# Kernel optimization log

Measured on AMD Instinct MI355X. Metric: run time of the kernel, lower is better.

The kernel has to match this reference:

```python
import jax, jax.numpy as jnp
import numpy as np

B, CIN, COUT, H, W = 4, 256, 256, 64, 64
K, G = 3, 4
PAD = (K - 1) // 2


def setup_inputs() -> dict:
    key = jax.random.key(0)
    k0, k1, k2, k3 = jax.random.split(key, 4)
    x = jax.random.normal(k0, (B, CIN, H, W), jnp.float32)
    y = jax.random.normal(k1, (B, 2, H, W), jnp.float32)
    # conv_offset: 1x1 conv, no bias, init std=0.1 (normal_init)
    w_offset = jax.random.normal(k2, (G * 2 * K * K, 2, 1, 1), jnp.float32) * 0.1
    # DeformConv2d weight, no bias, init std=0.01
    w_deform = jax.random.normal(k3, (COUT, CIN, K, K), jnp.float32) * 0.01
    return {"x": x, "y": y, "w_offset": w_offset, "w_deform": w_deform}


def _deform_conv(x, offset, weight):
    """DCN v1: stride 1, dilation 1, zero padding PAD, deform_groups=G, groups=1."""
    KK = K * K
    # mmcv offset layout: [B, G*2*KK, H, W] -> per group, per kernel pos, (dy, dx)
    off = offset.reshape(B, G, KK, 2, H, W)
    dy, dx = off[:, :, :, 0], off[:, :, :, 1]            # [B,G,KK,H,W]
    ii, jj = jnp.meshgrid(jnp.arange(K), jnp.arange(K), indexing="ij")
    ky = ii.reshape(KK).astype(x.dtype)                  # kernel row offsets
    kx = jj.reshape(KK).astype(x.dtype)                  # kernel col offsets
    base_y = jnp.arange(H, dtype=x.dtype)[None, :, None] - PAD + ky[:, None, None]  # [KK,H,1]
    base_x = jnp.arange(W, dtype=x.dtype)[None, None, :] - PAD + kx[:, None, None]  # [KK,1,W]
    yc = dy + base_y                                     # [B,G,KK,H,W]
    xc = dx + base_x

    Cg = CIN // G
    xg = x.reshape(B, G, Cg, H, W)

    def sample(xg1, yc1, xc1):
        # xg1 [Cg,H,W]; yc1/xc1 [KK,H,W] -> bilinear sample with zero padding
        y0 = jnp.floor(yc1)
        x0 = jnp.floor(xc1)
        wy = yc1 - y0
        wx = xc1 - x0
        y0i = y0.astype(jnp.int32)
        x0i = x0.astype(jnp.int32)

        def gather(yi, xi):
            valid = (yi >= 0) & (yi < H) & (xi >= 0) & (xi < W)
            v = xg1[:, jnp.clip(yi, 0, H - 1), jnp.clip(xi, 0, W - 1)]  # [Cg,KK,H,W]
            return v * valid[None].astype(xg1.dtype)

        v00 = gather(y0i, x0i)
        v01 = gather(y0i, x0i + 1)
        v10 = gather(y0i + 1, x0i)
        v11 = gather(y0i + 1, x0i + 1)
        return (v00 * (1 - wy) * (1 - wx) + v01 * (1 - wy) * wx
                + v10 * wy * (1 - wx) + v11 * wy * wx)

    sampled = jax.vmap(jax.vmap(sample))(xg, yc, xc)     # [B,G,Cg,KK,H,W]
    sampled = sampled.reshape(B, CIN, KK, H, W)
    wflat = weight.reshape(COUT, CIN, KK)
    return jnp.einsum("bckhw,ock->bohw", sampled, wflat)  # [B,COUT,H,W]


def reference(x, y, w_offset, w_deform):
    # offset = conv_offset(y.detach()), a 1x1 conv without bias
    y_det = jax.lax.stop_gradient(y)
    offset = jnp.einsum("bihw,oi->bohw", y_det, w_offset[:, :, 0, 0])
    out = _deform_conv(x, offset, w_deform)
    return jax.nn.relu(out)
```

## Files before the change

### kernel.cpp

```cpp
#include <hip/hip_runtime.h>
#include <cstddef>

#define B_    4
#define CIN_  256
#define COUT_ 256
#define H_    64
#define W_    64
#define KK_   9
#define G_    4
#define PAD_  1
#define TPX   64
#define NSL   9

#define WS_XT   0u
#define WS_WB   8388608u
#define WS_P23  9568256u

typedef short bf16x8 __attribute__((ext_vector_type(8)));
typedef float f32x4  __attribute__((ext_vector_type(4)));
typedef __attribute__((address_space(1))) const unsigned int* gptr_t;
typedef __attribute__((address_space(3))) unsigned int*       lptr_t;

__device__ __forceinline__ unsigned short f2bf(float v) {
    unsigned int u = __float_as_uint(v);
    u += 0x7fffu + ((u >> 16) & 1u);
    return (unsigned short)(u >> 16);
}
__device__ __forceinline__ float f_lo(unsigned int u) { return __uint_as_float(u << 16); }
__device__ __forceinline__ float f_hi(unsigned int u) { return __uint_as_float(u & 0xffff0000u); }

__global__ __launch_bounds__(256) void prep_kernel(const float* __restrict__ x,
                                                   const float* __restrict__ w,
                                                   unsigned short* __restrict__ xT,
                                                   unsigned short* __restrict__ wb) {
    const int tid = threadIdx.x;
    if (blockIdx.x < 512) {
        __shared__ unsigned short s[128][66];
        const int bh    = blockIdx.x >> 1;
        const int chalf = blockIdx.x & 1;
        const size_t src_base = ((size_t)(bh >> 6) * CIN_ + chalf * 128) * (H_ * W_) + (bh & 63) * W_;
        #pragma unroll 4
        for (int k = 0; k < 32; ++k) {
            int i = k * 256 + tid;
            int c = i >> 6, wq = i & 63;
            s[c][wq] = f2bf(x[src_base + (size_t)c * (H_ * W_) + wq]);
        }
        __syncthreads();
        #pragma unroll 4
        for (int k = 0; k < 16; ++k) {
            int j  = k * 256 + tid;
            int c2 = (j & 63) * 2, wq = j >> 6;
            unsigned int lo = s[c2][wq], hi = s[c2 + 1][wq];
            *(unsigned int*)(xT + ((size_t)bh * 64 + wq) * 256 + chalf * 128 + c2) = lo | (hi << 16);
        }
    } else {
        const int base = (blockIdx.x - 512) * 1024 + tid * 4;
        #pragma unroll
        for (int u = 0; u < 4; ++u) {
            int idx = base + u;
            int e   = idx & 7;
            int pos = (idx >> 3) & 7;
            int o   = (idx >> 6) & 255;
            int t   = idx >> 14;
            int g   = t / 9, kk = t - g * 9;
            int j   = pos ^ (o & 7);
            int c   = g * 64 + j * 8 + e;
            wb[idx] = f2bf(w[(o * CIN_ + c) * KK_ + kk]);
        }
    }
}

__global__ __launch_bounds__(512, 4) void dcn_kernel(
    const unsigned short* __restrict__ xT, const float* __restrict__ y,
    const float* __restrict__ w_off, const unsigned short* __restrict__ wb,
    unsigned int* __restrict__ outu,
    unsigned int* __restrict__ p23)
{
    __shared__ unsigned short s_W[COUT_ * 64];
    __shared__ unsigned short s_S[TPX * 64];

    const int tid = threadIdx.x;
    const int bid = blockIdx.x;
    const int kq  = bid & 3;
    const int bl  = (bid >> 2) & 1;
    const int loc = bid >> 3;
    const int h   = loc & 63;
    const int b   = (loc >> 6) * 2 + bl;

    const int sp = tid & 63;
    const int c8 = tid >> 6;

    const float yv0 = y[((b * 2 + 0) * H_ + h) * W_ + sp];
    const float yv1 = y[((b * 2 + 1) * H_ + h) * W_ + sp];

    const int lane = tid & 63, wave = tid >> 6;
    const int pg  = wave & 1, oh = wave >> 1;
    const int l15 = lane & 15, kq4 = lane >> 4, sw = l15 & 7;

    f32x4 acc[8];
    #pragma unroll
    for (int i = 0; i < 8; ++i) acc[i] = (f32x4){0.f, 0.f, 0.f, 0.f};

    const size_t xbase = (size_t)b * (H_ * W_ * 256) + c8 * 8;

    for (int sl = 0; sl < NSL; ++sl) {
        const int s  = kq * NSL + sl;
        const int kk = sl;

        __syncthreads();

        {
            const unsigned short* src = wb + (size_t)s * 16384;
            #pragma unroll
            for (int j = 0; j < 4; ++j) {
                const int off = (j * 512 + tid) * 8;
                __builtin_amdgcn_global_load_lds((gptr_t)(src + off),
                                                 (lptr_t)(s_W + off), 16, 0, 0);
            }
        }

        {
            const float4 co = *(const float4*)(w_off + s * 4);
            const float dy = fmaf(yv0, co.x, yv1 * co.y);
            const float dx = fmaf(yv0, co.z, yv1 * co.w);
            const float yc = (float)(h + (kk / 3) - PAD_) + dy;
            const float xc = (float)(sp + (kk % 3) - PAD_) + dx;
            const float yf = floorf(yc), xf = floorf(xc);
            const float wy = yc - yf,    wx = xc - xf;
            const int   yi = (int)yf,    xi = (int)xf;
            float w00 = (1.f - wy) * (1.f - wx);
            float w01 = (1.f - wy) * wx;
            float w10 = wy * (1.f - wx);
            float w11 = wy * wx;
            const bool y0ok = (yi >= 0) & (yi < H_);
            const bool y1ok = (yi >= -1) & (yi < H_ - 1);
            const bool x0ok = (xi >= 0) & (xi < W_);
            const bool x1ok = (xi >= -1) & (xi < W_ - 1);
            w00 = (y0ok & x0ok) ? w00 : 0.f;
            w01 = (y0ok & x1ok) ? w01 : 0.f;
            w10 = (y1ok & x0ok) ? w10 : 0.f;
            w11 = (y1ok & x1ok) ? w11 : 0.f;
            const int y0c = min(max(yi, 0), H_ - 1);
            const int y1c = min(max(yi + 1, 0), H_ - 1);
            const int x0c = min(max(xi, 0), W_ - 1);
            const int x1c = min(max(xi + 1, 0), W_ - 1);
            const unsigned short* xb = xT + xbase + kq * 64;
            const uint4 A  = *(const uint4*)(xb + ((size_t)y0c * W_ + x0c) * 256);
            const uint4 Bv = *(const uint4*)(xb + ((size_t)y0c * W_ + x1c) * 256);
            const uint4 C  = *(const uint4*)(xb + ((size_t)y1c * W_ + x0c) * 256);
            const uint4 D  = *(const uint4*)(xb + ((size_t)y1c * W_ + x1c) * 256);
            const unsigned int av[4] = {A.x, A.y, A.z, A.w};
            const unsigned int bv[4] = {Bv.x, Bv.y, Bv.z, Bv.w};
            const unsigned int cv[4] = {C.x, C.y, C.z, C.w};
            const unsigned int dv[4] = {D.x, D.y, D.z, D.w};
            unsigned int res[4];
            #pragma unroll
            for (int q = 0; q < 4; ++q) {
                float rl = w00 * f_lo(av[q]);
                rl = fmaf(w01, f_lo(bv[q]), rl);
                rl = fmaf(w10, f_lo(cv[q]), rl);
                rl = fmaf(w11, f_lo(dv[q]), rl);
                float rh = w00 * f_hi(av[q]);
                rh = fmaf(w01, f_hi(bv[q]), rh);
                rh = fmaf(w10, f_hi(cv[q]), rh);
                rh = fmaf(w11, f_hi(dv[q]), rh);
                res[q] = __builtin_amdgcn_perm(__float_as_uint(rh),
                                               __float_as_uint(rl), 0x07060302u);
            }
            *(uint4*)(s_S + sp * 64 + ((c8 ^ (sp & 7)) * 8)) =
                make_uint4(res[0], res[1], res[2], res[3]);
        }

        __syncthreads();

        bf16x8 bf[2][2], af[2][4];
        #pragma unroll
        for (int kh = 0; kh < 2; ++kh) {
            const int pos = ((kh * 4 + kq4) ^ sw) * 8;
            #pragma unroll
            for (int nt = 0; nt < 2; ++nt)
                bf[kh][nt] = *(const bf16x8*)(s_S + (pg * 32 + nt * 16 + l15) * 64 + pos);
            #pragma unroll
            for (int mt = 0; mt < 4; ++mt)
                af[kh][mt] = *(const bf16x8*)(s_W + (oh * 64 + mt * 16 + l15) * 64 + pos);
        }
        #pragma unroll
        for (int kh = 0; kh < 2; ++kh)
            #pragma unroll
            for (int nt = 0; nt < 2; ++nt)
                #pragma unroll
                for (int mt = 0; mt < 4; ++mt)
                    acc[nt * 4 + mt] = __builtin_amdgcn_mfma_f32_16x16x32_bf16(
                        af[kh][mt], bf[kh][nt], acc[nt * 4 + mt], 0, 0, 0);
    }

    unsigned short* pdst = (unsigned short*)((kq < 2) ? outu : p23) + (kq & 1);
    #pragma unroll
    for (int nt = 0; nt < 2; ++nt) {
        const int px = pg * 32 + nt * 16 + l15;
        #pragma unroll
        for (int mt = 0; mt < 4; ++mt) {
            const int obase = oh * 64 + mt * 16 + kq4 * 4;
            #pragma unroll
            for (int r = 0; r < 4; ++r) {
                const size_t gi = (((size_t)b * COUT_ + obase + r) * H_ + h) * W_ + px;
                pdst[gi * 2] = f2bf(acc[nt * 4 + mt][r]);
            }
        }
    }
}

__global__ __launch_bounds__(256) void red_kernel(const unsigned int* __restrict__ p23,
                                                  unsigned int* __restrict__ outu) {
    const size_t i = ((size_t)blockIdx.x * 256 + threadIdx.x) * 4;
    const uint4 a = *(const uint4*)(outu + i);
    const uint4 c = *(const uint4*)(p23 + i);
    float4 r;
    r.x = fmaxf(f_lo(a.x) + f_hi(a.x) + f_lo(c.x) + f_hi(c.x), 0.f);
    r.y = fmaxf(f_lo(a.y) + f_hi(a.y) + f_lo(c.y) + f_hi(c.y), 0.f);
    r.z = fmaxf(f_lo(a.z) + f_hi(a.z) + f_lo(c.z) + f_hi(c.z), 0.f);
    r.w = fmaxf(f_lo(a.w) + f_hi(a.w) + f_lo(c.w) + f_hi(c.w), 0.f);
    *(float4*)((float*)outu + i) = r;
}

extern "C" void kernel_launch(void* const* d_in, const int* in_sizes, int n_in,
                              void* d_out, int out_size, void* d_ws, size_t ws_size,
                              hipStream_t stream) {
    const float* x     = (const float*)d_in[0];
    const float* y     = (const float*)d_in[1];
    const float* w_off = (const float*)d_in[2];
    const float* w_def = (const float*)d_in[3];

    unsigned short* xT  = (unsigned short*)((char*)d_ws + WS_XT);
    unsigned short* wb  = (unsigned short*)((char*)d_ws + WS_WB);
    unsigned int*   p23 = (unsigned int*)((char*)d_ws + WS_P23);

    prep_kernel<<<1088, 256, 0, stream>>>(x, w_def, xT, wb);
    dcn_kernel<<<1024, 512, 0, stream>>>(xT, y, w_off, wb,
                                         (unsigned int*)d_out, p23);
    red_kernel<<<(B_ * COUT_ * H_ * W_) / 4 / 256, 256, 0, stream>>>(
        p23, (unsigned int*)d_out);
}
```

Measured before the change: 140.3 us.

## Double-buffer weight and sample LDS tiles to overlap loads with MFMA

After: 138.8 us. About the same (-1.1%).

```diff
diff --git a/kernel.cpp b/kernel.cpp
--- a/kernel.cpp
+++ b/kernel.cpp
@@ -70,14 +70,19 @@
     }
 }
 
+struct SampRegs {
+    uint4 A, Bv, C, D;
+    float w00, w01, w10, w11;
+};
+
 __global__ __launch_bounds__(512, 4) void dcn_kernel(
     const unsigned short* __restrict__ xT, const float* __restrict__ y,
     const float* __restrict__ w_off, const unsigned short* __restrict__ wb,
     unsigned int* __restrict__ outu,
     unsigned int* __restrict__ p23)
 {
-    __shared__ unsigned short s_W[COUT_ * 64];
-    __shared__ unsigned short s_S[TPX * 64];
+    __shared__ unsigned short s_W[2][COUT_ * 64];
+    __shared__ unsigned short s_S[2][TPX * 64];
 
     const int tid = threadIdx.x;
     const int bid = blockIdx.x;
@@ -103,95 +108,113 @@
 
     const size_t xbase = (size_t)b * (H_ * W_ * 256) + c8 * 8;
 
-    for (int sl = 0; sl < NSL; ++sl) {
+    auto dma_w = [&](int s, int buf) {
+        const unsigned short* src = wb + (size_t)s * 16384;
+        unsigned short* dst = &s_W[buf][0];
+        #pragma unroll
+        for (int j = 0; j < 4; ++j) {
+            const int off = (j * 512 + tid) * 8;
+            __builtin_amdgcn_global_load_lds((gptr_t)(src + off),
+                                             (lptr_t)(dst + off), 16, 0, 0);
+        }
+    };
+
+    auto sample_load = [&](int sl) -> SampRegs {
+        SampRegs r;
         const int s  = kq * NSL + sl;
         const int kk = sl;
-
-        __syncthreads();
-
-        {
-            const unsigned short* src = wb + (size_t)s * 16384;
-            #pragma unroll
-            for (int j = 0; j < 4; ++j) {
-                const int off = (j * 512 + tid) * 8;
-                __builtin_amdgcn_global_load_lds((gptr_t)(src + off),
-                                                 (lptr_t)(s_W + off), 16, 0, 0);
-            }
-        }
-
-        {
-            const float4 co = *(const float4*)(w_off + s * 4);
-            const float dy = fmaf(yv0, co.x, yv1 * co.y);
-            const float dx = fmaf(yv0, co.z, yv1 * co.w);
-            const float yc = (float)(h + (kk / 3) - PAD_) + dy;
-            const float xc = (float)(sp + (kk % 3) - PAD_) + dx;
-            const float yf = floorf(yc), xf = floorf(xc);
-            const float wy = yc - yf,    wx = xc - xf;
-            const int   yi = (int)yf,    xi = (int)xf;
-            float w00 = (1.f - wy) * (1.f - wx);
-            float w01 = (1.f - wy) * wx;
-            float w10 = wy * (1.f - wx);
-            float w11 = wy * wx;
-            const bool y0ok = (yi >= 0) & (yi < H_);
-            const bool y1ok = (yi >= -1) & (yi < H_ - 1);
-            const bool x0ok = (xi >= 0) & (xi < W_);
-            const bool x1ok = (xi >= -1) & (xi < W_ - 1);
-            w00 = (y0ok & x0ok) ? w00 : 0.f;
-            w01 = (y0ok & x1ok) ? w01 : 0.f;
-            w10 = (y1ok & x0ok) ? w10 : 0.f;
-            w11 = (y1ok & x1ok) ? w11 : 0.f;
-            const int y0c = min(max(yi, 0), H_ - 1);
-            const int y1c = min(max(yi + 1, 0), H_ - 1);
-            const int x0c = min(max(xi, 0), W_ - 1);
-            const int x1c = min(max(xi + 1, 0), W_ - 1);
-            const unsigned short* xb = xT + xbase + kq * 64;
-            const uint4 A  = *(const uint4*)(xb + ((size_t)y0c * W_ + x0c) * 256);
-            const uint4 Bv = *(const uint4*)(xb + ((size_t)y0c * W_ + x1c) * 256);
-            const uint4 C  = *(const uint4*)(xb + ((size_t)y1c * W_ + x0c) * 256);
-            const uint4 D  = *(const uint4*)(xb + ((size_t)y1c * W_ + x1c) * 256);
-            const unsigned int av[4] = {A.x, A.y, A.z, A.w};
-            const unsigned int bv[4] = {Bv.x, Bv.y, Bv.z, Bv.w};
-            const unsigned int cv[4] = {C.x, C.y, C.z, C.w};
-            const unsigned int dv[4] = {D.x, D.y, D.z, D.w};
-            unsigned int res[4];
-            #pragma unroll
-            for (int q = 0; q < 4; ++q) {
-                float rl = w00 * f_lo(av[q]);
-                rl = fmaf(w01, f_lo(bv[q]), rl);
-                rl = fmaf(w10, f_lo(cv[q]), rl);
-                rl = fmaf(w11, f_lo(dv[q]), rl);
-                float rh = w00 * f_hi(av[q]);
-                rh = fmaf(w01, f_hi(bv[q]), rh);
-                rh = fmaf(w10, f_hi(cv[q]), rh);
-                rh = fmaf(w11, f_hi(dv[q]), rh);
-                res[q] = __builtin_amdgcn_perm(__float_as_uint(rh),
-                                               __float_as_uint(rl), 0x07060302u);
-            }
-            *(uint4*)(s_S + sp * 64 + ((c8 ^ (sp & 7)) * 8)) =
-                make_uint4(res[0], res[1], res[2], res[3]);
-        }
-
-        __syncthreads();
-
-        bf16x8 bf[2][2], af[2][4];
+        const float4 co = *(const float4*)(w_off + s * 4);
+        const float dy = fmaf(yv0, co.x, yv1 * co.y);
+        const float dx = fmaf(yv0, co.z, yv1 * co.w);
+        const float yc = (float)(h + (kk / 3) - PAD_) + dy;
+        const float xc = (float)(sp + (kk % 3) - PAD_) + dx;
+        const float yf = floorf(yc), xf = floorf(xc);
+        const float wy = yc - yf,    wx = xc - xf;
+        const int   yi = (int)yf,    xi = (int)xf;
+        float w00 = (1.f - wy) * (1.f - wx);
+        float w01 = (1.f - wy) * wx;
+        float w10 = wy * (1.f - wx);
+        float w11 = wy * wx;
+        const bool y0ok = (yi >= 0) & (yi < H_);
+        const bool y1ok = (yi >= -1) & (yi < H_ - 1);
+        const bool x0ok = (xi >= 0) & (xi < W_);
+        const bool x1ok = (xi >= -1) & (xi < W_ - 1);
+        r.w00 = (y0ok & x0ok) ? w00 : 0.f;
+        r.w01 = (y0ok & x1ok) ? w01 : 0.f;
+        r.w10 = (y1ok & x0ok) ? w10 : 0.f;
+        r.w11 = (y1ok & x1ok) ? w11 : 0.f;
+        const int y0c = min(max(yi, 0), H_ - 1);
+        const int y1c = min(max(yi + 1, 0), H_ - 1);
+        const int x0c = min(max(xi, 0), W_ - 1);
+        const int x1c = min(max(xi + 1, 0), W_ - 1);
+        const unsigned short* xb = xT + xbase + kq * 64;
+        r.A  = *(const uint4*)(xb + ((size_t)y0c * W_ + x0c) * 256);
+        r.Bv = *(const uint4*)(xb + ((size_t)y0c * W_ + x1c) * 256);
+        r.C  = *(const uint4*)(xb + ((size_t)y1c * W_ + x0c) * 256);
+        r.D  = *(const uint4*)(xb + ((size_t)y1c * W_ + x1c) * 256);
+        return r;
+    };
+
+    auto sample_store = [&](const SampRegs& r, int buf) {
+        const unsigned int av[4] = {r.A.x, r.A.y, r.A.z, r.A.w};
+        const unsigned int bv[4] = {r.Bv.x, r.Bv.y, r.Bv.z, r.Bv.w};
+        const unsigned int cv[4] = {r.C.x, r.C.y, r.C.z, r.C.w};
+        const unsigned int dv[4] = {r.D.x, r.D.y, r.D.z, r.D.w};
+        unsigned int res[4];
+        #pragma unroll
+        for (int q = 0; q < 4; ++q) {
+            float rl = r.w00 * f_lo(av[q]);
+            rl = fmaf(r.w01, f_lo(bv[q]), rl);
+            rl = fmaf(r.w10, f_lo(cv[q]), rl);
+            rl = fmaf(r.w11, f_lo(dv[q]), rl);
+            float rh = r.w00 * f_hi(av[q]);
+            rh = fmaf(r.w01, f_hi(bv[q]), rh);
+            rh = fmaf(r.w10, f_hi(cv[q]), rh);
+            rh = fmaf(r.w11, f_hi(dv[q]), rh);
+            res[q] = __builtin_amdgcn_perm(__float_as_uint(rh),
+                                           __float_as_uint(rl), 0x07060302u);
+        }
+        *(uint4*)(&s_S[buf][0] + sp * 64 + ((c8 ^ (sp & 7)) * 8)) =
+            make_uint4(res[0], res[1], res[2], res[3]);
+    };
+
+    dma_w(kq * NSL, 0);
+    {
+        SampRegs r0 = sample_load(0);
+        sample_store(r0, 0);
+    }
+    __syncthreads();
+
+    for (int sl = 0; sl < NSL; ++sl) {
+        const int cur = sl & 1;
+        SampRegs rn;
+        if (sl < NSL - 1) {
+            dma_w(kq * NSL + sl + 1, cur ^ 1);
+            rn = sample_load(sl + 1);
+        }
+
+        const unsigned short* Wb = &s_W[cur][0];
+        const unsigned short* Sb = &s_S[cur][0];
         #pragma unroll
         for (int kh = 0; kh < 2; ++kh) {
             const int pos = ((kh * 4 + kq4) ^ sw) * 8;
+            bf16x8 bf[2], af[4];
             #pragma unroll
             for (int nt = 0; nt < 2; ++nt)
-                bf[kh][nt] = *(const bf16x8*)(s_S + (pg * 32 + nt * 16 + l15) * 64 + pos);
+                bf[nt] = *(const bf16x8*)(Sb + (pg * 32 + nt * 16 + l15) * 64 + pos);
             #pragma unroll
             for (int mt = 0; mt < 4; ++mt)
-                af[kh][mt] = *(const bf16x8*)(s_W + (oh * 64 + mt * 16 + l15) * 64 + pos);
-        }
-        #pragma unroll
-        for (int kh = 0; kh < 2; ++kh)
+                af[mt] = *(const bf16x8*)(Wb + (oh * 64 + mt * 16 + l15) * 64 + pos);
             #pragma unroll
             for (int nt = 0; nt < 2; ++nt)
                 #pragma unroll
                 for (int mt = 0; mt < 4; ++mt)
                     acc[nt * 4 + mt] = __builtin_amdgcn_mfma_f32_16x16x32_bf16(
-                        af[kh][mt], bf[kh][nt], acc[nt * 4 + mt], 0, 0, 0);
+                        af[mt], bf[nt], acc[nt * 4 + mt], 0, 0, 0);
+        }
+
+        if (sl < NSL - 1) sample_store(rn, cur ^ 1);
+        __syncthreads();
     }
 
     unsigned short* pdst = (unsigned short*)((kq < 2) ? outu : p23) + (kq & 1);
```
